# Performance work log

Measured on AMD Instinct MI355X. Metric: run time of the kernel, lower is better.

Reference implementation:

```python
import jax, jax.numpy as jnp
import numpy as np

B, C, N, K_NN = 16, 64, 2048, 3
OUT_C = 64


def setup_inputs() -> dict:
    key = jax.random.key(0)
    k1, k2, k3 = jax.random.split(key, 3)
    x = jax.random.normal(k1, (B, C, N), dtype=jnp.float32)
    fan_in = C * K_NN
    bound = 1.0 / np.sqrt(fan_in)
    W = jax.random.uniform(k2, (OUT_C, C, K_NN), minval=-bound, maxval=bound, dtype=jnp.float32)
    b = jax.random.uniform(k3, (OUT_C,), minval=-bound, maxval=bound, dtype=jnp.float32)
    return {"x": x, "W": W, "b": b}


def reference(x, W, b):
    # x: [B, C, N]; W: [O, C, K]; b: [O]
    K = W.shape[-1]
    # Pairwise squared distances: dist[b,i,j] = |x_i|^2 + |x_j|^2 - 2 x_i.x_j.
    # The original takes sqrt, but sqrt is monotone and the distances are only
    # used for top-k index selection, so we select on squared distances (same indices).
    norm_sq = jnp.sum(x * x, axis=1)                      # [B, N]
    dot = jnp.einsum('bcn,bcm->bnm', x, x)                # [B, N, N]
    dist_sq = norm_sq[:, :, None] + norm_sq[:, None, :] - 2.0 * dot  # [B, N, N]
    # K smallest distances per row -> neighbor indices [B, N, K]
    _, idx = jax.lax.top_k(-dist_sq, K)
    # Gather neighbors: neigh[b, c, n, k] = x[b, c, idx[b, n, k]]
    neigh = jax.vmap(lambda xb, ib: xb[:, ib])(x, idx)    # [B, C, N, K]
    # Conv1d with kernel_size == stride == K over the flattened [B, C, N*K]
    # tensor is exactly a per-window contraction over the K neighbors.
    out = jnp.einsum('bcnk,ock->bon', neigh, W) + b[None, :, None]  # [B, O, N]
    return out
```

## Files before the change

### kernel.cpp

```cpp
#include <hip/hip_runtime.h>
#include <cfloat>
#include <climits>

#define B_DIM 16
#define C_DIM 64
#define N_DIM 2048
#define O_DIM 64
#define K_NN  3

typedef __attribute__((ext_vector_type(8))) short bf16x8;
typedef __attribute__((ext_vector_type(4))) float floatx4;

#define GLDS16(gsrc, ldst)                                        \
  __builtin_amdgcn_global_load_lds(                               \
      (const __attribute__((address_space(1))) void*)(gsrc),      \
      (__attribute__((address_space(3))) void*)(ldst), 16, 0, 0)

__device__ __forceinline__ unsigned short f32_to_bf16_rne(float f) {
  unsigned int u = __float_as_uint(f);
  return (unsigned short)((u + 0x7fffu + ((u >> 16) & 1u)) >> 16);
}
__device__ __forceinline__ float bf16_to_f32(unsigned short h) {
  return __uint_as_float(((unsigned int)h) << 16);
}

__device__ __forceinline__ unsigned med3u(unsigned a, unsigned b, unsigned c) {
  unsigned mn = min(a, b), mx = max(a, b);
  return max(mn, min(mx, c));
}

__device__ __forceinline__ void ins4p(unsigned u, int jv, unsigned* k, int* j) {
  bool c3 = u < k[3], c2 = u < k[2], c1 = u < k[1], c0 = u < k[0];
  k[3] = c2 ? k[2] : (c3 ? u  : k[3]);
  j[3] = c2 ? j[2] : (c3 ? jv : j[3]);
  k[2] = c1 ? k[1] : (c2 ? u  : k[2]);
  j[2] = c1 ? j[1] : (c2 ? jv : j[2]);
  k[1] = c0 ? k[0] : (c1 ? u  : k[1]);
  j[1] = c0 ? j[0] : (c1 ? jv : j[1]);
  k[0] = c0 ? u  : k[0];
  j[0] = c0 ? jv : j[0];
}

__global__ __launch_bounds__(256) void prep_kernel(
    const float* __restrict__ x, float* __restrict__ xT,
    unsigned short* __restrict__ xTh, unsigned short* __restrict__ xTl,
    double* __restrict__ nd, float* __restrict__ nf,
    const float* __restrict__ W, float* __restrict__ Wt) {
  int bid = blockIdx.x;
  int t = threadIdx.x;
  if (bid >= 512) {
    int t2 = (bid - 512) * 256 + t;
    int o  = t2 / (C_DIM * K_NN);
    int ck = t2 - o * (C_DIM * K_NN);
    Wt[ck * O_DIM + o] = W[t2];
    return;
  }
  __shared__ __align__(16) float xs[C_DIM][68];
  int b  = bid >> 5;
  int n0 = (bid & 31) * 64;
  const float* xb = x + (size_t)b * C_DIM * N_DIM;
  #pragma unroll
  for (int r = 0; r < 4; ++r) {
    int idx = r * 256 + t;
    int c = idx >> 4;
    int qq = idx & 15;
    *(float4*)&xs[c][qq * 4] = *(const float4*)(xb + (size_t)c * N_DIM + n0 + qq * 4);
  }
  __syncthreads();
  int n = t >> 2, cg = t & 3;
  float v[16];
  #pragma unroll
  for (int cc = 0; cc < 16; ++cc) v[cc] = xs[cg * 16 + cc][n];
  double ps = 0.0;
  #pragma unroll
  for (int cc = 0; cc < 16; ++cc) ps = fma((double)v[cc], (double)v[cc], ps);
  ps += __shfl_xor(ps, 1, 64);
  ps += __shfl_xor(ps, 2, 64);
  size_t row = (size_t)b * N_DIM + n0 + n;
  #pragma unroll
  for (int qq = 0; qq < 4; ++qq) {
    float4 wv; wv.x = v[qq*4]; wv.y = v[qq*4+1]; wv.z = v[qq*4+2]; wv.w = v[qq*4+3];
    *(float4*)&xT[row * C_DIM + cg * 16 + qq * 4] = wv;
  }
  unsigned short hh[16], ll[16];
  #pragma unroll
  for (int cc = 0; cc < 16; ++cc) {
    hh[cc] = f32_to_bf16_rne(v[cc]);
    ll[cc] = f32_to_bf16_rne(v[cc] - bf16_to_f32(hh[cc]));
  }
  #pragma unroll
  for (int e = 0; e < 2; ++e) {
    int phys = (2 * cg + e) ^ (n & 7);
    unsigned int hp[4], lp[4];
    #pragma unroll
    for (int xk = 0; xk < 4; ++xk) {
      hp[xk] = (unsigned)hh[e*8 + 2*xk] | ((unsigned)hh[e*8 + 2*xk + 1] << 16);
      lp[xk] = (unsigned)ll[e*8 + 2*xk] | ((unsigned)ll[e*8 + 2*xk + 1] << 16);
    }
    ((uint4*)xTh)[row * 8 + phys] = *(uint4*)hp;
    ((uint4*)xTl)[row * 8 + phys] = *(uint4*)lp;
  }
  if (cg == 0) {
    nd[row] = ps;
    nf[row] = (float)ps + 512.0f;
  }
}

__global__ __launch_bounds__(256, 2) void topk_kernel(
    const unsigned short* __restrict__ xTh, const unsigned short* __restrict__ xTl,
    const float* __restrict__ nf, unsigned short* __restrict__ cand) {
  __shared__ __align__(16) unsigned short Jh[2][128 * 64];
  __shared__ __align__(16) unsigned short Jl[2][128 * 64];
  int bid   = blockIdx.x;
  int q     = bid & 3;
  int itile = (bid >> 2) & 31;
  int b     = bid >> 7;
  int i0    = itile * 64;
  int jq0   = q * 512;
  int t = threadIdx.x;
  int w = t >> 6, lane = t & 63, quad = lane >> 4, col = lane & 15;
  int csw = col & 7;
  const unsigned short* xh = xTh + (size_t)b * N_DIM * 64;
  const unsigned short* xl = xTl + (size_t)b * N_DIM * 64;
  const float* nfb = nf + b * N_DIM;

  bf16x8 ih[2], il[2];
  #pragma unroll
  for (int ks = 0; ks < 2; ++ks) {
    size_t row = i0 + w * 16 + col;
    int phys = (ks * 4 + quad) ^ csw;
    ih[ks] = *(const bf16x8*)(xh + row * 64 + phys * 8);
    il[ks] = *(const bf16x8*)(xl + row * 64 + phys * 8);
  }

  unsigned ck[4];
  ck[0] = ck[1] = ck[2] = ck[3] = 0xFFFFFFFFu;

  int a0 = col * 64 + ((quad ^ csw) * 8);
  int a1 = col * 64 + (((4 + quad) ^ csw) * 8);

  const unsigned short* sbh = xh + (size_t)(jq0 + w * 32) * 64 + lane * 8;
  const unsigned short* sbl = xl + (size_t)(jq0 + w * 32) * 64 + lane * 8;
  int ldsb = w * 32 * 64;

  #pragma unroll
  for (int k2 = 0; k2 < 4; ++k2) {
    GLDS16(sbh + k2 * 512, &Jh[0][ldsb + k2 * 512]);
    GLDS16(sbl + k2 * 512, &Jl[0][ldsb + k2 * 512]);
  }
  __syncthreads();

  #pragma unroll
  for (int js = 0; js < 4; ++js) {
    int cur = js & 1, nxt = cur ^ 1;
    int j0 = jq0 + js * 128;

    if (js < 3) {
      #pragma unroll
      for (int k2 = 0; k2 < 4; ++k2) {
        GLDS16(sbh + (js + 1) * 8192 + k2 * 512, &Jh[nxt][ldsb + k2 * 512]);
        GLDS16(sbl + (js + 1) * 8192 + k2 * 512, &Jl[nxt][ldsb + k2 * 512]);
      }
    }

    floatx4 acc[8];
    #pragma unroll
    for (int jt = 0; jt < 8; ++jt) acc[jt] = (floatx4){0.f, 0.f, 0.f, 0.f};

    #pragma unroll
    for (int ks = 0; ks < 2; ++ks) {
      int ab = ks ? a1 : a0;
      #pragma unroll
      for (int jt = 0; jt < 8; ++jt) {
        bf16x8 jh = *(const bf16x8*)&Jh[cur][jt * 1024 + ab];
        bf16x8 jl = *(const bf16x8*)&Jl[cur][jt * 1024 + ab];
        acc[jt] = __builtin_amdgcn_mfma_f32_16x16x32_bf16(jl, ih[ks], acc[jt], 0, 0, 0);
        acc[jt] = __builtin_amdgcn_mfma_f32_16x16x32_bf16(jh, il[ks], acc[jt], 0, 0, 0);
        acc[jt] = __builtin_amdgcn_mfma_f32_16x16x32_bf16(jh, ih[ks], acc[jt], 0, 0, 0);
      }
    }

    unsigned locb = (unsigned)(js << 5);
    int jb = j0 + quad * 4;
    #pragma unroll
    for (int jt = 0; jt < 8; ++jt) {
      float4 nv = *(const float4*)(nfb + jb + jt * 16);
      float nfa[4] = {nv.x, nv.y, nv.z, nv.w};
      #pragma unroll
      for (int r = 0; r < 4; ++r) {
        float key = fmaf(-2.0f, acc[jt][r], nfa[r]);
        unsigned u = (__float_as_uint(key) & 0xFFFFFF80u) | locb |
                     (unsigned)(jt * 4 + r);
        unsigned m0 = min(ck[0], u);
        unsigned m1 = med3u(ck[0], u, ck[1]);
        unsigned m2 = med3u(ck[1], u, ck[2]);
        unsigned m3 = med3u(ck[2], u, ck[3]);
        ck[0] = m0; ck[1] = m1; ck[2] = m2; ck[3] = m3;
      }
    }

    __syncthreads();
  }

  int cj[4];
  #pragma unroll
  for (int s = 0; s < 4; ++s) {
    unsigned loc = ck[s] & 127u;
    cj[s] = jq0 + (int)((loc >> 5) << 7) + (int)(((loc >> 2) & 7u) << 4) +
            (quad << 2) + (int)(loc & 3u);
  }
  #pragma unroll
  for (int m = 16; m < 64; m <<= 1) {
    unsigned tu[4]; int tj[4];
    #pragma unroll
    for (int s = 0; s < 4; ++s) {
      tu[s] = __shfl_xor(ck[s], m, 64);
      tj[s] = __shfl_xor(cj[s], m, 64);
    }
    #pragma unroll
    for (int s = 0; s < 4; ++s) ins4p(tu[s], tj[s], ck, cj);
  }
  if (quad == 0) {
    int row = b * N_DIM + i0 + w * 16 + col;
    unsigned short* cp = cand + row * 16 + q * 4;
    cp[0] = (unsigned short)cj[0];
    cp[1] = (unsigned short)cj[1];
    cp[2] = (unsigned short)cj[2];
    cp[3] = (unsigned short)cj[3];
  }
}

#define NT   64
#define NPAD 68
__global__ __launch_bounds__(256) void conv_kernel(
    const float* __restrict__ xT, const double* __restrict__ nd,
    const unsigned short* __restrict__ cand,
    const float* __restrict__ Wt, const float* __restrict__ bias,
    float* __restrict__ out) {
  __shared__ __align__(16) float nb[C_DIM * K_NN][NPAD];
  __shared__ unsigned short tks[NT][4];
  int bid = blockIdx.x;
  int b  = bid >> 5;
  int n0 = (bid & 31) * NT;
  const float* xtb = xT + (size_t)b * N_DIM * C_DIM;
  int t = threadIdx.x;
  int w = t >> 6, lane = t & 63;
  int cid = lane >> 2, seg = lane & 3;

  for (int it = 0; it < 16; ++it) {
    int nn = w * 16 + it;
    int row = b * N_DIM + n0 + nn;
    int j = cand[row * 16 + cid];
    const float* xn = xtb + ((size_t)(n0 + nn) * C_DIM) + seg * 16;
    const float* xj = xtb + ((size_t)j * C_DIM) + seg * 16;
    double pd = 0.0;
    #pragma unroll
    for (int qq = 0; qq < 4; ++qq) {
      float4 a  = *(const float4*)(xn + qq * 4);
      float4 bb = *(const float4*)(xj + qq * 4);
      pd = fma((double)a.x, (double)bb.x, pd);
      pd = fma((double)a.y, (double)bb.y, pd);
      pd = fma((double)a.z, (double)bb.z, pd);
      pd = fma((double)a.w, (double)bb.w, pd);
    }
    pd += __shfl_xor(pd, 1, 64);
    pd += __shfl_xor(pd, 2, 64);
    double key = fma(-2.0, pd, nd[b * N_DIM + j] + 512.0);
    unsigned long long u =
        ((unsigned long long)__double_as_longlong(key) & ~2047ull) |
        (unsigned long long)(unsigned)j;
    unsigned long long v = u;
    #pragma unroll
    for (int p = 0; p < 3; ++p) {
      unsigned long long m = v;
      #pragma unroll
      for (int msk = 4; msk < 64; msk <<= 1) {
        unsigned long long o = __shfl_xor(m, msk, 64);
        m = (o < m) ? o : m;
      }
      if (lane == 0) tks[nn][p] = (unsigned short)(m & 2047ull);
      v = (v == m) ? ~0ull : v;
    }
  }
  __syncthreads();

  #pragma unroll
  for (int p = 0; p < 12; ++p) {
    int u = p * 256 + t;
    int sg = u & 15;
    int r  = u >> 4;
    int k = r >> 6, n = r & 63;
    int j = tks[n][k];
    float4 v = *(const float4*)(xtb + (size_t)j * C_DIM + sg * 4);
    nb[(sg * 4 + 0) * 3 + k][n] = v.x;
    nb[(sg * 4 + 1) * 3 + k][n] = v.y;
    nb[(sg * 4 + 2) * 3 + k][n] = v.z;
    nb[(sg * 4 + 3) * 3 + k][n] = v.w;
  }
  __syncthreads();

  int ng = t & 15, og = t >> 4;
  float acc[4][4];
  #pragma unroll
  for (int oo = 0; oo < 4; ++oo) {
    float bv = bias[(og << 2) + oo];
    #pragma unroll
    for (int nn2 = 0; nn2 < 4; ++nn2) acc[oo][nn2] = bv;
  }
  const float* nbp = &nb[0][0] + (ng << 2);
  const float* wtp = Wt + (og << 2);
  #pragma unroll 4
  for (int ckk = 0; ckk < C_DIM * K_NN; ++ckk) {
    float4 nv = *(const float4*)(nbp + ckk * NPAD);
    float4 wv = *(const float4*)(wtp + ckk * O_DIM);
    float na[4] = {nv.x, nv.y, nv.z, nv.w};
    float wa[4] = {wv.x, wv.y, wv.z, wv.w};
    #pragma unroll
    for (int oo = 0; oo < 4; ++oo)
      #pragma unroll
      for (int nn2 = 0; nn2 < 4; ++nn2)
        acc[oo][nn2] = fmaf(wa[oo], na[nn2], acc[oo][nn2]);
  }
  #pragma unroll
  for (int oo = 0; oo < 4; ++oo) {
    int o = (og << 2) + oo;
    float4 v; v.x = acc[oo][0]; v.y = acc[oo][1]; v.z = acc[oo][2]; v.w = acc[oo][3];
    *(float4*)&out[(size_t)(b * O_DIM + o) * N_DIM + n0 + (ng << 2)] = v;
  }
}

extern "C" void kernel_launch(void* const* d_in, const int* in_sizes, int n_in,
                              void* d_out, int out_size, void* d_ws, size_t ws_size,
                              hipStream_t stream) {
  const float* x    = (const float*)d_in[0];
  const float* W    = (const float*)d_in[1];
  const float* bias = (const float*)d_in[2];
  float* out = (float*)d_out;
  char* ws = (char*)d_ws;
  float*          xT  = (float*)ws;
  unsigned short* xTh = (unsigned short*)(ws + 8388608);
  unsigned short* xTl = (unsigned short*)(ws + 12582912);
  double*         nd  = (double*)(ws + 16777216);
  float*          nfp = (float*)(ws + 17039360);
  unsigned short* cd  = (unsigned short*)(ws + 17170432);
  float*          Wt  = (float*)(ws + 18219008);

  prep_kernel<<<512 + 48, 256, 0, stream>>>(x, xT, xTh, xTl, nd, nfp, W, Wt);
  topk_kernel<<<B_DIM * 32 * 4, 256, 0, stream>>>(xTh, xTl, nfp, cd);
  conv_kernel<<<B_DIM * (N_DIM / NT), 256, 0, stream>>>(xT, nd, cd, Wt, bias, out);
}
```

Measured before the change: 155.3 us.

## Retile topk kernel to 128 query rows per block with smaller j-chunks

```diff
diff --git a/kernel.cpp b/kernel.cpp
--- a/kernel.cpp
+++ b/kernel.cpp
@@ -106,16 +106,16 @@
   }
 }
 
-__global__ __launch_bounds__(256, 2) void topk_kernel(
+__global__ __launch_bounds__(256, 4) void topk_kernel(
     const unsigned short* __restrict__ xTh, const unsigned short* __restrict__ xTl,
     const float* __restrict__ nf, unsigned short* __restrict__ cand) {
-  __shared__ __align__(16) unsigned short Jh[2][128 * 64];
-  __shared__ __align__(16) unsigned short Jl[2][128 * 64];
+  __shared__ __align__(16) unsigned short Jh[2][64 * 64];
+  __shared__ __align__(16) unsigned short Jl[2][64 * 64];
   int bid   = blockIdx.x;
   int q     = bid & 3;
-  int itile = (bid >> 2) & 31;
-  int b     = bid >> 7;
-  int i0    = itile * 64;
+  int itile = (bid >> 2) & 15;
+  int b     = bid >> 6;
+  int i0    = itile * 128;
   int jq0   = q * 512;
   int t = threadIdx.x;
   int w = t >> 6, lane = t & 63, quad = lane >> 4, col = lane & 15;
@@ -124,109 +124,127 @@
   const unsigned short* xl = xTl + (size_t)b * N_DIM * 64;
   const float* nfb = nf + b * N_DIM;
 
-  bf16x8 ih[2], il[2];
-  #pragma unroll
-  for (int ks = 0; ks < 2; ++ks) {
-    size_t row = i0 + w * 16 + col;
-    int phys = (ks * 4 + quad) ^ csw;
-    ih[ks] = *(const bf16x8*)(xh + row * 64 + phys * 8);
-    il[ks] = *(const bf16x8*)(xl + row * 64 + phys * 8);
-  }
-
-  unsigned ck[4];
-  ck[0] = ck[1] = ck[2] = ck[3] = 0xFFFFFFFFu;
+  bf16x8 ih[2][2], il[2][2];
+  #pragma unroll
+  for (int s2 = 0; s2 < 2; ++s2) {
+    #pragma unroll
+    for (int ks = 0; ks < 2; ++ks) {
+      size_t row = i0 + w * 32 + s2 * 16 + col;
+      int phys = (ks * 4 + quad) ^ csw;
+      ih[s2][ks] = *(const bf16x8*)(xh + row * 64 + phys * 8);
+      il[s2][ks] = *(const bf16x8*)(xl + row * 64 + phys * 8);
+    }
+  }
+
+  unsigned ck[2][4];
+  #pragma unroll
+  for (int s2 = 0; s2 < 2; ++s2)
+    ck[s2][0] = ck[s2][1] = ck[s2][2] = ck[s2][3] = 0xFFFFFFFFu;
 
   int a0 = col * 64 + ((quad ^ csw) * 8);
   int a1 = col * 64 + (((4 + quad) ^ csw) * 8);
 
-  const unsigned short* sbh = xh + (size_t)(jq0 + w * 32) * 64 + lane * 8;
-  const unsigned short* sbl = xl + (size_t)(jq0 + w * 32) * 64 + lane * 8;
-  int ldsb = w * 32 * 64;
-
-  #pragma unroll
-  for (int k2 = 0; k2 < 4; ++k2) {
+  const unsigned short* sbh = xh + (size_t)(jq0 + w * 16) * 64 + lane * 8;
+  const unsigned short* sbl = xl + (size_t)(jq0 + w * 16) * 64 + lane * 8;
+  int ldsb = w * 16 * 64;
+
+  #pragma unroll
+  for (int k2 = 0; k2 < 2; ++k2) {
     GLDS16(sbh + k2 * 512, &Jh[0][ldsb + k2 * 512]);
     GLDS16(sbl + k2 * 512, &Jl[0][ldsb + k2 * 512]);
   }
   __syncthreads();
 
   #pragma unroll
-  for (int js = 0; js < 4; ++js) {
+  for (int js = 0; js < 8; ++js) {
     int cur = js & 1, nxt = cur ^ 1;
-    int j0 = jq0 + js * 128;
-
-    if (js < 3) {
-      #pragma unroll
-      for (int k2 = 0; k2 < 4; ++k2) {
-        GLDS16(sbh + (js + 1) * 8192 + k2 * 512, &Jh[nxt][ldsb + k2 * 512]);
-        GLDS16(sbl + (js + 1) * 8192 + k2 * 512, &Jl[nxt][ldsb + k2 * 512]);
-      }
-    }
-
-    floatx4 acc[8];
-    #pragma unroll
-    for (int jt = 0; jt < 8; ++jt) acc[jt] = (floatx4){0.f, 0.f, 0.f, 0.f};
+    int j0 = jq0 + js * 64;
+
+    if (js < 7) {
+      #pragma unroll
+      for (int k2 = 0; k2 < 2; ++k2) {
+        GLDS16(sbh + (js + 1) * 4096 + k2 * 512, &Jh[nxt][ldsb + k2 * 512]);
+        GLDS16(sbl + (js + 1) * 4096 + k2 * 512, &Jl[nxt][ldsb + k2 * 512]);
+      }
+    }
+
+    floatx4 acc[2][4];
+    #pragma unroll
+    for (int s2 = 0; s2 < 2; ++s2)
+      #pragma unroll
+      for (int jt = 0; jt < 4; ++jt) acc[s2][jt] = (floatx4){0.f, 0.f, 0.f, 0.f};
 
     #pragma unroll
     for (int ks = 0; ks < 2; ++ks) {
       int ab = ks ? a1 : a0;
       #pragma unroll
-      for (int jt = 0; jt < 8; ++jt) {
+      for (int jt = 0; jt < 4; ++jt) {
         bf16x8 jh = *(const bf16x8*)&Jh[cur][jt * 1024 + ab];
         bf16x8 jl = *(const bf16x8*)&Jl[cur][jt * 1024 + ab];
-        acc[jt] = __builtin_amdgcn_mfma_f32_16x16x32_bf16(jl, ih[ks], acc[jt], 0, 0, 0);
-        acc[jt] = __builtin_amdgcn_mfma_f32_16x16x32_bf16(jh, il[ks], acc[jt], 0, 0, 0);
-        acc[jt] = __builtin_amdgcn_mfma_f32_16x16x32_bf16(jh, ih[ks], acc[jt], 0, 0, 0);
-      }
-    }
-
-    unsigned locb = (unsigned)(js << 5);
+        #pragma unroll
+        for (int s2 = 0; s2 < 2; ++s2) {
+          acc[s2][jt] = __builtin_amdgcn_mfma_f32_16x16x32_bf16(jl, ih[s2][ks], acc[s2][jt], 0, 0, 0);
+          acc[s2][jt] = __builtin_amdgcn_mfma_f32_16x16x32_bf16(jh, il[s2][ks], acc[s2][jt], 0, 0, 0);
+          acc[s2][jt] = __builtin_amdgcn_mfma_f32_16x16x32_bf16(jh, ih[s2][ks], acc[s2][jt], 0, 0, 0);
+        }
+      }
+    }
+
+    unsigned locb = (unsigned)(js << 4);
     int jb = j0 + quad * 4;
     #pragma unroll
-    for (int jt = 0; jt < 8; ++jt) {
+    for (int jt = 0; jt < 4; ++jt) {
       float4 nv = *(const float4*)(nfb + jb + jt * 16);
       float nfa[4] = {nv.x, nv.y, nv.z, nv.w};
       #pragma unroll
       for (int r = 0; r < 4; ++r) {
-        float key = fmaf(-2.0f, acc[jt][r], nfa[r]);
-        unsigned u = (__float_as_uint(key) & 0xFFFFFF80u) | locb |
-                     (unsigned)(jt * 4 + r);
-        unsigned m0 = min(ck[0], u);
-        unsigned m1 = med3u(ck[0], u, ck[1]);
-        unsigned m2 = med3u(ck[1], u, ck[2]);
-        unsigned m3 = med3u(ck[2], u, ck[3]);
-        ck[0] = m0; ck[1] = m1; ck[2] = m2; ck[3] = m3;
+        unsigned idbits = locb | (unsigned)(jt * 4 + r);
+        #pragma unroll
+        for (int s2 = 0; s2 < 2; ++s2) {
+          float key = fmaf(-2.0f, acc[s2][jt][r], nfa[r]);
+          unsigned u = (__float_as_uint(key) & 0xFFFFFF80u) | idbits;
+          unsigned m0 = min(ck[s2][0], u);
+          unsigned m1 = med3u(ck[s2][0], u, ck[s2][1]);
+          unsigned m2 = med3u(ck[s2][1], u, ck[s2][2]);
+          unsigned m3 = med3u(ck[s2][2], u, ck[s2][3]);
+          ck[s2][0] = m0; ck[s2][1] = m1; ck[s2][2] = m2; ck[s2][3] = m3;
+        }
       }
     }
 
     __syncthreads();
   }
 
-  int cj[4];
-  #pragma unroll
-  for (int s = 0; s < 4; ++s) {
-    unsigned loc = ck[s] & 127u;
-    cj[s] = jq0 + (int)((loc >> 5) << 7) + (int)(((loc >> 2) & 7u) << 4) +
-            (quad << 2) + (int)(loc & 3u);
-  }
-  #pragma unroll
-  for (int m = 16; m < 64; m <<= 1) {
-    unsigned tu[4]; int tj[4];
+  #pragma unroll
+  for (int s2 = 0; s2 < 2; ++s2) {
+    int cj[4];
+    unsigned cku[4];
     #pragma unroll
     for (int s = 0; s < 4; ++s) {
-      tu[s] = __shfl_xor(ck[s], m, 64);
-      tj[s] = __shfl_xor(cj[s], m, 64);
-    }
-    #pragma unroll
-    for (int s = 0; s < 4; ++s) ins4p(tu[s], tj[s], ck, cj);
-  }
-  if (quad == 0) {
-    int row = b * N_DIM + i0 + w * 16 + col;
-    unsigned short* cp = cand + row * 16 + q * 4;
-    cp[0] = (unsigned short)cj[0];
-    cp[1] = (unsigned short)cj[1];
-    cp[2] = (unsigned short)cj[2];
-    cp[3] = (unsigned short)cj[3];
+      unsigned loc = ck[s2][s] & 127u;
+      cj[s] = jq0 + (int)((loc >> 4) << 6) + (int)(((loc >> 2) & 3u) << 4) +
+              (quad << 2) + (int)(loc & 3u);
+      cku[s] = ck[s2][s];
+    }
+    #pragma unroll
+    for (int m = 16; m < 64; m <<= 1) {
+      unsigned tu[4]; int tj[4];
+      #pragma unroll
+      for (int s = 0; s < 4; ++s) {
+        tu[s] = __shfl_xor(cku[s], m, 64);
+        tj[s] = __shfl_xor(cj[s], m, 64);
+      }
+      #pragma unroll
+      for (int s = 0; s < 4; ++s) ins4p(tu[s], tj[s], cku, cj);
+    }
+    if (quad == 0) {
+      int row = b * N_DIM + i0 + w * 32 + s2 * 16 + col;
+      unsigned short* cp = cand + row * 16 + q * 4;
+      cp[0] = (unsigned short)cj[0];
+      cp[1] = (unsigned short)cj[1];
+      cp[2] = (unsigned short)cj[2];
+      cp[3] = (unsigned short)cj[3];
+    }
   }
 }
 
@@ -346,6 +364,6 @@
   float*          Wt  = (float*)(ws + 18219008);
 
   prep_kernel<<<512 + 48, 256, 0, stream>>>(x, xT, xTh, xTl, nd, nfp, W, Wt);
-  topk_kernel<<<B_DIM * 32 * 4, 256, 0, stream>>>(xTh, xTl, nfp, cd);
+  topk_kernel<<<B_DIM * 16 * 4, 256, 0, stream>>>(xTh, xTl, nfp, cd);
   conv_kernel<<<B_DIM * (N_DIM / NT), 256, 0, stream>>>(xT, nd, cd, Wt, bias, out);
 }
```

After: 144.6 us. 1.07x faster.
